# Kernel tuning notes

Hardware: AMD Instinct MI355X
Metric: run time of the kernel (lower is better)

## Reference

```python
import jax, jax.numpy as jnp
import numpy as np

N = 12        # ALL_QUBITS
COM_Q = 9     # COM_QUBITS
IMG_Q = 11    # IMG_QUBITS
LAYERS = 2
SQRT2 = float(np.sqrt(2.0))
H_GATE = jnp.asarray([[1.0, 1.0], [1.0, -1.0]], dtype=jnp.complex64) / SQRT2


def _bitrev_perm(q):
    # column j of the wires-1..q subspace corresponds to param index bitrev(j)
    idx = np.arange(2 ** q)
    rev = np.zeros_like(idx)
    for bpos in range(q):
        rev |= ((idx >> bpos) & 1) << (q - 1 - bpos)
    return rev


def _apply_1q(state, U, w):
    # state: (B, 2^N) complex; apply 2x2 gate U on wire w (wire 0 = MSB)
    B = state.shape[0]
    s = state.reshape(B, 2 ** w, 2, -1)
    return jnp.einsum('ij,bpjq->bpiq', U, s).reshape(B, -1)


def _apply_cnot(state, c, t):
    B = state.shape[0]
    s = state.reshape((B,) + (2,) * N)
    s0 = jax.lax.slice_in_dim(s, 0, 1, axis=c + 1)
    s1 = jnp.flip(jax.lax.slice_in_dim(s, 1, 2, axis=c + 1), axis=t + 1)
    return jnp.concatenate([s0, s1], axis=c + 1).reshape(B, -1)


def _frqi(state, angles, q):
    # Hadamards on wires 1..q, then uniformly-controlled RY(angles) on wire 0
    for w in range(1, q + 1):
        state = _apply_1q(state, H_GATE, w)
    rev = _bitrev_perm(q)
    half = 0.5 * angles[:, rev]            # (B, 2^q), angle per control column
    c = jnp.cos(half)[:, :, None]
    s = jnp.sin(half)[:, :, None]
    B = state.shape[0]
    st = state.reshape(B, 2, 2 ** q, -1)   # (B, wire0, wires1..q, rest)
    new0 = c * st[:, 0] - s * st[:, 1]
    new1 = s * st[:, 0] + c * st[:, 1]
    return jnp.stack([new0, new1], axis=1).reshape(B, -1)


def _rot(phi, theta, omega):
    # PennyLane Rot = RZ(omega) RY(theta) RZ(phi)
    c = jnp.cos(theta / 2)
    s = jnp.sin(theta / 2)
    m00 = jnp.exp(-0.5j * (phi + omega)) * c
    m01 = -jnp.exp(0.5j * (phi - omega)) * s
    m10 = jnp.exp(-0.5j * (phi - omega)) * s
    m11 = jnp.exp(0.5j * (phi + omega)) * c
    return jnp.stack([jnp.stack([m00, m01]), jnp.stack([m10, m11])])


def _circuit(com_params, img_params, qp):
    B = com_params.shape[0]
    state = jnp.zeros((B, 2 ** N), jnp.complex64).at[:, 0].set(1.0)
    state = _frqi(state, com_params, COM_Q)
    for l in range(LAYERS):  # StronglyEntanglingLayers
        for w in range(N):
            state = _apply_1q(state, _rot(qp[l, w, 0], qp[l, w, 1], qp[l, w, 2]), w)
        r = l % (N - 1) + 1  # default ranges
        for w in range(N):
            state = _apply_cnot(state, w, (w + r) % N)
    state = _frqi(state, img_params, IMG_Q)
    p = (jnp.abs(state.reshape(B, 2, -1)) ** 2).sum(axis=2)  # (B, 2) wire-0 probs
    return p[:, 1] - p[:, 0]  # expval of Hamiltonian = -1 * Z(0)


def setup_inputs() -> dict:
    key = jax.random.key(0)
    k1, k2, k3 = jax.random.split(key, 3)
    B = 1024
    x = jax.random.uniform(k1, (B, 2, 32, 32), dtype=jnp.float32)
    W = jax.random.normal(k2, (512, 2048), dtype=jnp.float32) * 0.02
    b = jnp.zeros((512,), dtype=jnp.float32)
    quantum_params = jax.random.uniform(k3, (LAYERS, N, 3), dtype=jnp.float32) * float(np.pi)
    return {"x": x, "W": W, "b": b, "quantum_params": quantum_params}


def reference(x, W, b, quantum_params):
    B = x.shape[0]
    xf = x.reshape(B, -1)                 # (B, 2048) img_params
    com = xf @ W.T + b                    # (B, 512) classical_nn output
    return _circuit(com, xf, quantum_params)
```

## Files before the change

kernel.cpp:

```cpp
#include <hip/hip_runtime.h>
#include <math.h>

#define RS2f 0.70710678118654752f

typedef __attribute__((ext_vector_type(8))) short bf16x8;
typedef __attribute__((ext_vector_type(4))) float f32x4;

__device__ __forceinline__ unsigned short f2bf(float f) {
    unsigned u = __float_as_uint(f);
    unsigned r = (u + 0x7fffu + ((u >> 16) & 1u)) >> 16;
    return (unsigned short)r;
}
__device__ __forceinline__ float bf2f(unsigned short h) {
    return __uint_as_float(((unsigned)h) << 16);
}

__global__ __launch_bounds__(256) void split_all(const float* __restrict__ x,
                                                 const float* __restrict__ W,
                                                 unsigned short* __restrict__ xc,
                                                 unsigned short* __restrict__ wc) {
    int idx = blockIdx.x * 256 + threadIdx.x;
    const float* src; unsigned short* dst;
    if (idx < 524288) { src = x; dst = xc; }
    else              { idx -= 524288; src = W; dst = wc; }
    int m = idx >> 9;
    int c4 = (idx & 511) << 2;
    const float4 v = *(const float4*)&src[m * 2048 + c4];
    ushort4 hi, lo;
    hi.x = f2bf(v.x); lo.x = f2bf(v.x - bf2f(hi.x));
    hi.y = f2bf(v.y); lo.y = f2bf(v.y - bf2f(hi.y));
    hi.z = f2bf(v.z); lo.z = f2bf(v.z - bf2f(hi.z));
    hi.w = f2bf(v.w); lo.w = f2bf(v.w - bf2f(hi.w));
    *(ushort4*)&dst[m * 4096 + c4] = hi;
    *(ushort4*)&dst[m * 4096 + 2048 + c4] = lo;
}

__global__ __launch_bounds__(256) void gemm64(const unsigned short* __restrict__ A,
                                              const unsigned short* __restrict__ B,
                                              float* __restrict__ P, int nch) {
    __shared__ short As[64 * 72];
    __shared__ short Bs[64 * 72];
    const int tid = threadIdx.x, lane = tid & 63, wv = tid >> 6;
    const int quad = lane >> 4, mrow = lane & 15;
    const int m0 = blockIdx.x * 64, n0 = blockIdx.y * 64;
    const int kb = blockIdx.z * nch * 64;
    const int srow = tid >> 2;
    const int sk = (tid & 3) * 16;
    const unsigned short* Arow = A + (size_t)(m0 + srow) * 4096 + kb + sk;
    const unsigned short* Brow = B + (size_t)(n0 + srow) * 4096 + kb + sk;

    f32x4 acc[4];
    #pragma unroll
    for (int j = 0; j < 4; ++j) acc[j] = (f32x4){0.f, 0.f, 0.f, 0.f};

    float4 a0 = *(const float4*)Arow;
    float4 a1 = *(const float4*)(Arow + 8);
    float4 b0 = *(const float4*)Brow;
    float4 b1 = *(const float4*)(Brow + 8);

    for (int ch = 0; ch < nch; ++ch) {
        __syncthreads();
        *(float4*)&As[srow * 72 + sk]     = a0;
        *(float4*)&As[srow * 72 + sk + 8] = a1;
        *(float4*)&Bs[srow * 72 + sk]     = b0;
        *(float4*)&Bs[srow * 72 + sk + 8] = b1;
        __syncthreads();
        if (ch + 1 < nch) {
            const int o = (ch + 1) * 64;
            a0 = *(const float4*)(Arow + o);
            a1 = *(const float4*)(Arow + o + 8);
            b0 = *(const float4*)(Brow + o);
            b1 = *(const float4*)(Brow + o + 8);
        }
        #pragma unroll
        for (int ks = 0; ks < 2; ++ks) {
            bf16x8 af = *(const bf16x8*)&As[(wv * 16 + mrow) * 72 + ks * 32 + quad * 8];
            #pragma unroll
            for (int j = 0; j < 4; ++j) {
                bf16x8 bf = *(const bf16x8*)&Bs[(j * 16 + mrow) * 72 + ks * 32 + quad * 8];
                acc[j] = __builtin_amdgcn_mfma_f32_16x16x32_bf16(af, bf, acc[j], 0, 0, 0);
            }
        }
    }
    float* Pz = P + (size_t)blockIdx.z * 524288;
    #pragma unroll
    for (int j = 0; j < 4; ++j)
        #pragma unroll
        for (int r = 0; r < 4; ++r)
            Pz[(m0 + wv * 16 + quad * 4 + r) * 512 + n0 + j * 16 + mrow] = acc[j][r];
}

__global__ __launch_bounds__(256) void gemm_f32(const float* __restrict__ A,
                                                const float* __restrict__ W,
                                                float* __restrict__ P) {
    __shared__ float Asf[32][128];
    __shared__ float Bsf[32][128];
    const int tid = threadIdx.x;
    const int m0 = blockIdx.x * 128;
    const int n0 = blockIdx.y * 128;
    const int kchunk = 2048 / gridDim.z;
    const int kbase = blockIdx.z * kchunk;
    const int tm = tid >> 4, tn = tid & 15;
    const int srow = tid >> 1;
    const int scol = (tid & 1) * 16;
    float acc[8][8] = {};
    for (int k0 = kbase; k0 < kbase + kchunk; k0 += 32) {
        float4 a[4], w[4];
        const float4* Ap = (const float4*)&A[(m0 + srow) * 2048 + k0 + scol];
        const float4* Wp = (const float4*)&W[(n0 + srow) * 2048 + k0 + scol];
        #pragma unroll
        for (int q = 0; q < 4; ++q) { a[q] = Ap[q]; w[q] = Wp[q]; }
        __syncthreads();
        #pragma unroll
        for (int q = 0; q < 4; ++q) {
            Asf[scol + 4*q + 0][srow] = a[q].x; Asf[scol + 4*q + 1][srow] = a[q].y;
            Asf[scol + 4*q + 2][srow] = a[q].z; Asf[scol + 4*q + 3][srow] = a[q].w;
            Bsf[scol + 4*q + 0][srow] = w[q].x; Bsf[scol + 4*q + 1][srow] = w[q].y;
            Bsf[scol + 4*q + 2][srow] = w[q].z; Bsf[scol + 4*q + 3][srow] = w[q].w;
        }
        __syncthreads();
        #pragma unroll
        for (int kk = 0; kk < 32; ++kk) {
            float4 af0 = *(const float4*)&Asf[kk][tm * 8];
            float4 af1 = *(const float4*)&Asf[kk][tm * 8 + 4];
            float4 bf0 = *(const float4*)&Bsf[kk][tn * 8];
            float4 bf1 = *(const float4*)&Bsf[kk][tn * 8 + 4];
            float av[8] = {af0.x,af0.y,af0.z,af0.w,af1.x,af1.y,af1.z,af1.w};
            float bv[8] = {bf0.x,bf0.y,bf0.z,bf0.w,bf1.x,bf1.y,bf1.z,bf1.w};
            #pragma unroll
            for (int r = 0; r < 8; ++r)
                #pragma unroll
                for (int c = 0; c < 8; ++c)
                    acc[r][c] += av[r] * bv[c];
        }
    }
    float* Pz = P + (size_t)blockIdx.z * 524288;
    #pragma unroll
    for (int r = 0; r < 8; ++r) {
        float4 lo = make_float4(acc[r][0], acc[r][1], acc[r][2], acc[r][3]);
        float4 hi = make_float4(acc[r][4], acc[r][5], acc[r][6], acc[r][7]);
        float* dst = &Pz[(m0 + tm*8 + r) * 512 + n0 + tn*8];
        *(float4*)dst = lo;
        *(float4*)(dst + 4) = hi;
    }
}

struct CMat { float m00r,m00i,m01r,m01i,m10r,m10i,m11r,m11i; };

__device__ __forceinline__ CMat mk_rot(const float* __restrict__ qp, int l, int w) {
    const float* g = qp + (l * 12 + w) * 3;
    float phi = g[0], th = g[1], om = g[2];
    float st, ct, sa, ca, sb, cb;
    sincosf(0.5f * th, &st, &ct);
    sincosf(0.5f * (phi + om), &sa, &ca);
    sincosf(0.5f * (phi - om), &sb, &cb);
    CMat M;
    M.m00r =  ct * ca; M.m00i = -ct * sa;
    M.m01r = -st * cb; M.m01i = -st * sb;
    M.m10r =  st * cb; M.m10i = -st * sb;
    M.m11r =  ct * ca; M.m11i =  ct * sa;
    return M;
}

template<int W> struct WI {
    static constexpr int kind = (W == 0 || W == 7) ? 2 : ((W >= 1 && W <= 6) ? 1 : 0);
    static constexpr int eb   = (W >= 8) ? (11 - W) : 0;
    static constexpr int lm   = (W >= 1 && W <= 6) ? (1 << (6 - W)) : 0;
    static constexpr int vm   = (W == 0) ? 2 : ((W == 7) ? 1 : 0);
};

__device__ __forceinline__ void exch_put(float* xbuf, int slot,
                                         const float vr[16], const float vi[16]) {
    __syncthreads();
    float4* p = (float4*)xbuf;
    #pragma unroll
    for (int j = 0; j < 8; ++j)
        p[(j << 8) + slot] = make_float4(vr[2*j], vi[2*j], vr[2*j+1], vi[2*j+1]);
    __syncthreads();
}

__device__ __forceinline__ void shfl_perm(float vr[16], float vi[16], int src) {
    #pragma unroll
    for (int e = 0; e < 16; ++e) {
        vr[e] = __shfl(vr[e], src, 64);
        vi[e] = __shfl(vi[e], src, 64);
    }
}

template<int EB>
__device__ __forceinline__ void rot_local(float vr[16], float vi[16], const CMat& M) {
    #pragma unroll
    for (int e = 0; e < 16; ++e) if (!(e & (1 << EB))) {
        const int e1 = e | (1 << EB);
        float x0r = vr[e],  x0i = vi[e];
        float x1r = vr[e1], x1i = vi[e1];
        vr[e]  = M.m00r*x0r - M.m00i*x0i + M.m01r*x1r - M.m01i*x1i;
        vi[e]  = M.m00r*x0i + M.m00i*x0r + M.m01r*x1i + M.m01i*x1r;
        vr[e1] = M.m10r*x0r - M.m10i*x0i + M.m11r*x1r - M.m11i*x1i;
        vi[e1] = M.m10r*x0i + M.m10i*x0r + M.m11r*x1i + M.m11i*x1r;
    }
}

template<int LM>
__device__ __forceinline__ void rot_lane(float vr[16], float vi[16], int lane, const CMat& M) {
    const bool hi = lane & LM;
    const float Ar = hi ? M.m11r : M.m00r, Ai = hi ? M.m11i : M.m00i;
    const float Br = hi ? M.m10r : M.m01r, Bi = hi ? M.m10i : M.m01i;
    #pragma unroll
    for (int e = 0; e < 16; ++e) {
        float pr = __shfl_xor(vr[e], LM, 64);
        float pi = __shfl_xor(vi[e], LM, 64);
        float orr = vr[e], oi = vi[e];
        vr[e] = Ar*orr - Ai*oi + Br*pr - Bi*pi;
        vi[e] = Ar*oi + Ai*orr + Br*pi + Bi*pr;
    }
}

template<int VM>
__device__ __forceinline__ void rot_wave(float vr[16], float vi[16], float* xbuf,
                                         int waveId, int lane, const CMat& M) {
    exch_put(xbuf, (waveId << 6) + lane, vr, vi);
    const float4* p = (const float4*)xbuf;
    const int ps = ((waveId ^ VM) << 6) + lane;
    const bool hi = waveId & VM;
    const float Ar = hi ? M.m11r : M.m00r, Ai = hi ? M.m11i : M.m00i;
    const float Br = hi ? M.m10r : M.m01r, Bi = hi ? M.m10i : M.m01i;
    #pragma unroll
    for (int j = 0; j < 8; ++j) {
        float4 q = p[(j << 8) + ps];
        const int e0 = 2*j, e1 = 2*j + 1;
        float r0 = vr[e0], i0 = vi[e0], r1 = vr[e1], i1 = vi[e1];
        vr[e0] = Ar*r0 - Ai*i0 + Br*q.x - Bi*q.y;
        vi[e0] = Ar*i0 + Ai*r0 + Br*q.y + Bi*q.x;
        vr[e1] = Ar*r1 - Ai*i1 + Br*q.z - Bi*q.w;
        vi[e1] = Ar*i1 + Ai*r1 + Br*q.w + Bi*q.z;
    }
}

template<int W>
__device__ __forceinline__ void rot_wire(float vr[16], float vi[16], float* xbuf,
                                         int waveId, int lane, const CMat& M) {
    if constexpr (WI<W>::kind == 0)      rot_local<WI<W>::eb>(vr, vi, M);
    else if constexpr (WI<W>::kind == 1) rot_lane<WI<W>::lm>(vr, vi, lane, M);
    else                                 rot_wave<WI<W>::vm>(vr, vi, xbuf, waveId, lane, M);
}

template<int C, int T>
__device__ __forceinline__ void cnot(float vr[16], float vi[16], float* xbuf,
                                     int waveId, int lane) {
    constexpr int ck = WI<C>::kind, tk = WI<T>::kind;
    if constexpr (ck == 0 && tk == 0) {
        constexpr int cb = 1 << WI<C>::eb, tb = 1 << WI<T>::eb;
        #pragma unroll
        for (int e = 0; e < 16; ++e) if ((e & cb) && !(e & tb)) {
            const int e1 = e | tb;
            float t = vr[e]; vr[e] = vr[e1]; vr[e1] = t;
            t = vi[e]; vi[e] = vi[e1]; vi[e1] = t;
        }
    } else if constexpr (ck == 0 && tk == 1) {
        constexpr int cb = 1 << WI<C>::eb, tm = WI<T>::lm;
        #pragma unroll
        for (int e = 0; e < 16; ++e) if (e & cb) {
            vr[e] = __shfl_xor(vr[e], tm, 64);
            vi[e] = __shfl_xor(vi[e], tm, 64);
        }
    } else if constexpr (ck == 0 && tk == 2) {
        constexpr int cb = 1 << WI<C>::eb, vm = WI<T>::vm;
        exch_put(xbuf, (waveId << 6) + lane, vr, vi);
        const float4* p = (const float4*)xbuf;
        const int ps = ((waveId ^ vm) << 6) + lane;
        #pragma unroll
        for (int j = 0; j < 8; ++j) {
            if ((((2*j) & cb) != 0) || (((2*j+1) & cb) != 0)) {
                float4 q = p[(j << 8) + ps];
                if (((2*j) & cb) != 0)   { vr[2*j]   = q.x; vi[2*j]   = q.y; }
                if (((2*j+1) & cb) != 0) { vr[2*j+1] = q.z; vi[2*j+1] = q.w; }
            }
        }
    } else if constexpr (ck == 1 && tk == 0) {
        constexpr int cm = WI<C>::lm, tb = 1 << WI<T>::eb;
        const bool cc = lane & cm;
        #pragma unroll
        for (int e = 0; e < 16; ++e) if (!(e & tb)) {
            const int e1 = e | tb;
            float a = vr[e], bb = vr[e1];
            vr[e] = cc ? bb : a; vr[e1] = cc ? a : bb;
            a = vi[e]; bb = vi[e1];
            vi[e] = cc ? bb : a; vi[e1] = cc ? a : bb;
        }
    } else if constexpr (ck == 1 && tk == 1) {
        constexpr int cm = WI<C>::lm, tm = WI<T>::lm;
        const int src = (lane & cm) ? (lane ^ tm) : lane;
        shfl_perm(vr, vi, src);
    } else if constexpr (ck == 1 && tk == 2) {
        constexpr int cm = WI<C>::lm, vm = WI<T>::vm;
        exch_put(xbuf, (waveId << 6) + lane, vr, vi);
        const float4* p = (const float4*)xbuf;
        const int ps = ((waveId ^ vm) << 6) + lane;
        const bool take = lane & cm;
        #pragma unroll
        for (int j = 0; j < 8; ++j) {
            float4 q = p[(j << 8) + ps];
            vr[2*j]   = take ? q.x : vr[2*j];   vi[2*j]   = take ? q.y : vi[2*j];
            vr[2*j+1] = take ? q.z : vr[2*j+1]; vi[2*j+1] = take ? q.w : vi[2*j+1];
        }
    } else if constexpr (ck == 2 && tk == 0) {
        constexpr int vm = WI<C>::vm, tb = 1 << WI<T>::eb;
        if (waveId & vm) {
            #pragma unroll
            for (int e = 0; e < 16; ++e) if (!(e & tb)) {
                const int e1 = e | tb;
                float t = vr[e]; vr[e] = vr[e1]; vr[e1] = t;
                t = vi[e]; vi[e] = vi[e1]; vi[e1] = t;
            }
        }
    } else {
        constexpr int vm = WI<C>::vm, tm = WI<T>::lm;
        if (waveId & vm) {
            #pragma unroll
            for (int e = 0; e < 16; ++e) {
                vr[e] = __shfl_xor(vr[e], tm, 64);
                vi[e] = __shfl_xor(vi[e], tm, 64);
            }
        }
    }
}

template<int W>
__device__ __forceinline__ void h_wire(float vr[16], float vi[16], float* xbuf,
                                       int waveId, int lane) {
    if constexpr (WI<W>::kind == 0) {
        constexpr int tb = 1 << WI<W>::eb;
        #pragma unroll
        for (int e = 0; e < 16; ++e) if (!(e & tb)) {
            const int e1 = e | tb;
            float x0 = vr[e], x1 = vr[e1];
            vr[e] = (x0 + x1) * RS2f; vr[e1] = (x0 - x1) * RS2f;
            x0 = vi[e]; x1 = vi[e1];
            vi[e] = (x0 + x1) * RS2f; vi[e1] = (x0 - x1) * RS2f;
        }
    } else if constexpr (WI<W>::kind == 1) {
        constexpr int m = WI<W>::lm;
        const float sgn = (lane & m) ? -RS2f : RS2f;
        #pragma unroll
        for (int e = 0; e < 16; ++e) {
            float pr = __shfl_xor(vr[e], m, 64);
            float pi = __shfl_xor(vi[e], m, 64);
            vr[e] = pr * RS2f + vr[e] * sgn;
            vi[e] = pi * RS2f + vi[e] * sgn;
        }
    } else {
        constexpr int vm = WI<W>::vm;
        exch_put(xbuf, (waveId << 6) + lane, vr, vi);
        const float4* p = (const float4*)xbuf;
        const int ps = ((waveId ^ vm) << 6) + lane;
        const float sgn = (waveId & vm) ? -RS2f : RS2f;
        #pragma unroll
        for (int j = 0; j < 8; ++j) {
            float4 q = p[(j << 8) + ps];
            vr[2*j]   = q.x * RS2f + vr[2*j]   * sgn;
            vi[2*j]   = q.y * RS2f + vi[2*j]   * sgn;
            vr[2*j+1] = q.z * RS2f + vr[2*j+1] * sgn;
            vi[2*j+1] = q.w * RS2f + vi[2*j+1] * sgn;
        }
    }
}

__global__ __launch_bounds__(256) void circuit_kernel(const float* __restrict__ P,
                                                      const float* __restrict__ bias,
                                                      const float* __restrict__ xf,
                                                      const float* __restrict__ qp,
                                                      float* __restrict__ out, int SK) {
    __shared__ float xbuf[8192];
    __shared__ float ang[2048];
    const int tid = threadIdx.x;
    const int lane = tid & 63;
    const int waveId = tid >> 6;
    const int b = blockIdx.x;

    if (tid < 128) {
        float4 s = ((const float4*)bias)[tid];
        for (int z = 0; z < SK; ++z) {
            float4 p4 = *(const float4*)&P[(size_t)z * 524288 + b * 512 + tid * 4];
            s.x += p4.x; s.y += p4.y; s.z += p4.z; s.w += p4.w;
        }
        ((float4*)ang)[tid] = s;
    }
    __syncthreads();

    float vr[16], vi[16];
    #pragma unroll
    for (int e = 0; e < 16; ++e) { vr[e] = 0.0f; vi[e] = 0.0f; }

    const float K9 = 0.044194173824159216f;
    #pragma unroll
    for (int m = 0; m < 4; ++m) {
        int j = (lane << 3) | ((waveId & 1) << 2) | m;
        int rj = (int)(__brev((unsigned)j) >> 23);
        float s, c;
        sincosf(0.5f * ang[rj], &s, &c);
        vr[m << 2] = K9 * ((waveId & 2) ? s : c);
    }

    #pragma unroll 1
    for (int l = 0; l < 2; ++l) {
        { CMat M = mk_rot(qp, l, 0);  rot_wire<0 >(vr, vi, xbuf, waveId, lane, M); }
        { CMat M = mk_rot(qp, l, 1);  rot_wire<1 >(vr, vi, xbuf, waveId, lane, M); }
        { CMat M = mk_rot(qp, l, 2);  rot_wire<2 >(vr, vi, xbuf, waveId, lane, M); }
        { CMat M = mk_rot(qp, l, 3);  rot_wire<3 >(vr, vi, xbuf, waveId, lane, M); }
        { CMat M = mk_rot(qp, l, 4);  rot_wire<4 >(vr, vi, xbuf, waveId, lane, M); }
        { CMat M = mk_rot(qp, l, 5);  rot_wire<5 >(vr, vi, xbuf, waveId, lane, M); }
        { CMat M = mk_rot(qp, l, 6);  rot_wire<6 >(vr, vi, xbuf, waveId, lane, M); }
        { CMat M = mk_rot(qp, l, 7);  rot_wire<7 >(vr, vi, xbuf, waveId, lane, M); }
        { CMat M = mk_rot(qp, l, 8);  rot_wire<8 >(vr, vi, xbuf, waveId, lane, M); }
        { CMat M = mk_rot(qp, l, 9);  rot_wire<9 >(vr, vi, xbuf, waveId, lane, M); }
        { CMat M = mk_rot(qp, l, 10); rot_wire<10>(vr, vi, xbuf, waveId, lane, M); }
        { CMat M = mk_rot(qp, l, 11); rot_wire<11>(vr, vi, xbuf, waveId, lane, M); }
        if (l == 0) {
            int j = lane;
            j ^= (j & 2)  ? 1  : 0;
            j ^= (j & 4)  ? 2  : 0;
            j ^= (j & 8)  ? 4  : 0;
            j ^= (j & 16) ? 8  : 0;
            j ^= (j & 32) ? 16 : 0;
            j ^= (waveId & 2) ? 32 : 0;
            shfl_perm(vr, vi, j);
            cnot<6,7>(vr,vi,xbuf,waveId,lane);   cnot<7,8>(vr,vi,xbuf,waveId,lane);
            cnot<8,9>(vr,vi,xbuf,waveId,lane);   cnot<9,10>(vr,vi,xbuf,waveId,lane);
            cnot<10,11>(vr,vi,xbuf,waveId,lane); cnot<11,0>(vr,vi,xbuf,waveId,lane);
        } else {
            int j = lane;
            j ^= (j & 4)  ? 1  : 0;
            j ^= (j & 8)  ? 2  : 0;
            j ^= (j & 16) ? 4  : 0;
            j ^= (j & 32) ? 8  : 0;
            j ^= (waveId & 2) ? 16 : 0;
            shfl_perm(vr, vi, j);
            cnot<5,7>(vr,vi,xbuf,waveId,lane);   cnot<6,8>(vr,vi,xbuf,waveId,lane);
            cnot<7,9>(vr,vi,xbuf,waveId,lane);   cnot<8,10>(vr,vi,xbuf,waveId,lane);
            cnot<9,11>(vr,vi,xbuf,waveId,lane);  cnot<10,0>(vr,vi,xbuf,waveId,lane);
            cnot<11,1>(vr,vi,xbuf,waveId,lane);
        }
    }

    h_wire<1>(vr,vi,xbuf,waveId,lane);  h_wire<2>(vr,vi,xbuf,waveId,lane);
    h_wire<3>(vr,vi,xbuf,waveId,lane);  h_wire<4>(vr,vi,xbuf,waveId,lane);
    h_wire<5>(vr,vi,xbuf,waveId,lane);  h_wire<6>(vr,vi,xbuf,waveId,lane);
    h_wire<7>(vr,vi,xbuf,waveId,lane);  h_wire<8>(vr,vi,xbuf,waveId,lane);
    h_wire<9>(vr,vi,xbuf,waveId,lane);  h_wire<10>(vr,vi,xbuf,waveId,lane);
    h_wire<11>(vr,vi,xbuf,waveId,lane);

    {
        const float4* x4 = (const float4*)(xf + b * 2048);
        ((float4*)ang)[tid]       = x4[tid];
        ((float4*)ang)[tid + 256] = x4[tid + 256];
    }
    __syncthreads();

    exch_put(xbuf, (waveId << 6) + lane, vr, vi);
    {
        const float4* p = (const float4*)xbuf;
        const int ps = ((waveId ^ 2) << 6) + lane;
        const bool hi = waveId & 2;
        float acc = 0.0f;
        #pragma unroll
        for (int j = 0; j < 8; ++j) {
            float4 q = p[(j << 8) + ps];
            #pragma unroll
            for (int h = 0; h < 2; ++h) {
                const int e = 2*j + h;
                const float prr = h ? q.z : q.x;
                const float pii = h ? q.w : q.y;
                int v = (lane << 5) | ((waveId & 1) << 4) | e;
                int rv = (int)(__brev((unsigned)v) >> 21);
                float s, c;
                sincosf(0.5f * ang[rv], &s, &c);
                float nr = hi ? (s*prr + c*vr[e]) : (c*vr[e] - s*prr);
                float ni = hi ? (s*pii + c*vi[e]) : (c*vi[e] - s*pii);
                acc += nr*nr + ni*ni;
            }
        }
        if (!hi) acc = -acc;
        #pragma unroll
        for (int off = 32; off > 0; off >>= 1) acc += __shfl_down(acc, off, 64);
        __syncthreads();
        if (lane == 0) xbuf[waveId] = acc;
        __syncthreads();
        if (tid == 0) out[b] = xbuf[0] + xbuf[1] + xbuf[2] + xbuf[3];
    }
}

extern "C" void kernel_launch(void* const* d_in, const int* in_sizes, int n_in,
                              void* d_out, int out_size, void* d_ws, size_t ws_size,
                              hipStream_t stream) {
    const float* x    = (const float*)d_in[0];
    const float* W    = (const float*)d_in[1];
    const float* bias = (const float*)d_in[2];
    const float* qp   = (const float*)d_in[3];
    float* out = (float*)d_out;

    const size_t MB = 1024ull * 1024;
    const size_t BASE = 12 * MB;
    if (ws_size >= BASE + 4 * MB) {
        unsigned short* xc = (unsigned short*)d_ws;
        unsigned short* wc = (unsigned short*)((char*)d_ws + 8 * MB);
        float* P = (float*)((char*)d_ws + BASE);
        int SK;
        if      (ws_size >= BASE + 16 * MB) SK = 8;
        else if (ws_size >= BASE + 8 * MB)  SK = 4;
        else                                SK = 2;
        split_all<<<3072, 256, 0, stream>>>(x, W, xc, wc);
        dim3 g(16, 8, SK);
        gemm64<<<g, 256, 0, stream>>>(xc, wc, P, 4096 / SK / 64);
        circuit_kernel<<<1024, 256, 0, stream>>>(P, bias, x, qp, out, SK);
    } else {
        float* P = (float*)d_ws;
        const size_t slab = 1024 * 512 * sizeof(float);
        int SK = 1;
        if      (ws_size >= 16 * slab) SK = 16;
        else if (ws_size >=  8 * slab) SK = 8;
        else if (ws_size >=  4 * slab) SK = 4;
        else if (ws_size >=  2 * slab) SK = 2;
        dim3 ggrid(8, 4, SK);
        gemm_f32<<<ggrid, 256, 0, stream>>>(x, W, P);
        circuit_kernel<<<1024, 256, 0, stream>>>(P, bias, x, qp, out, SK);
    }
}
```

Measured before the change: 150.5 us.

## Fuse split, GEMM and circuit into one cooperative persistent kernel

Merges the bf16 split conversion, the split-K MFMA GEMM and the per-sample circuit simulation into a single cooperative kernel, separated by grid-wide syncs, with shared memory reused across the phases. Split-K is fixed at 4 and work is distributed with grid-stride loops over 256 or 512 blocks, chosen from the occupancy query. The goal is to remove the launch gaps between three kernels. In exchange it adds grid barrier costs, and the circuit phase now runs on fewer resident blocks than the original 1024. The fallback path is rewritten as a smaller fp32 GEMM that adds the bias, followed by a standalone circuit kernel.

```diff
diff --git a/kernel.cpp b/kernel.cpp
--- a/kernel.cpp
+++ b/kernel.cpp
@@ -1,5 +1,8 @@
 #include <hip/hip_runtime.h>
+#include <hip/hip_cooperative_groups.h>
 #include <math.h>
+
+namespace cg = cooperative_groups;
 
 #define RS2f 0.70710678118654752f
 
@@ -13,136 +16,6 @@
 }
 __device__ __forceinline__ float bf2f(unsigned short h) {
     return __uint_as_float(((unsigned)h) << 16);
-}
-
-__global__ __launch_bounds__(256) void split_all(const float* __restrict__ x,
-                                                 const float* __restrict__ W,
-                                                 unsigned short* __restrict__ xc,
-                                                 unsigned short* __restrict__ wc) {
-    int idx = blockIdx.x * 256 + threadIdx.x;
-    const float* src; unsigned short* dst;
-    if (idx < 524288) { src = x; dst = xc; }
-    else              { idx -= 524288; src = W; dst = wc; }
-    int m = idx >> 9;
-    int c4 = (idx & 511) << 2;
-    const float4 v = *(const float4*)&src[m * 2048 + c4];
-    ushort4 hi, lo;
-    hi.x = f2bf(v.x); lo.x = f2bf(v.x - bf2f(hi.x));
-    hi.y = f2bf(v.y); lo.y = f2bf(v.y - bf2f(hi.y));
-    hi.z = f2bf(v.z); lo.z = f2bf(v.z - bf2f(hi.z));
-    hi.w = f2bf(v.w); lo.w = f2bf(v.w - bf2f(hi.w));
-    *(ushort4*)&dst[m * 4096 + c4] = hi;
-    *(ushort4*)&dst[m * 4096 + 2048 + c4] = lo;
-}
-
-__global__ __launch_bounds__(256) void gemm64(const unsigned short* __restrict__ A,
-                                              const unsigned short* __restrict__ B,
-                                              float* __restrict__ P, int nch) {
-    __shared__ short As[64 * 72];
-    __shared__ short Bs[64 * 72];
-    const int tid = threadIdx.x, lane = tid & 63, wv = tid >> 6;
-    const int quad = lane >> 4, mrow = lane & 15;
-    const int m0 = blockIdx.x * 64, n0 = blockIdx.y * 64;
-    const int kb = blockIdx.z * nch * 64;
-    const int srow = tid >> 2;
-    const int sk = (tid & 3) * 16;
-    const unsigned short* Arow = A + (size_t)(m0 + srow) * 4096 + kb + sk;
-    const unsigned short* Brow = B + (size_t)(n0 + srow) * 4096 + kb + sk;
-
-    f32x4 acc[4];
-    #pragma unroll
-    for (int j = 0; j < 4; ++j) acc[j] = (f32x4){0.f, 0.f, 0.f, 0.f};
-
-    float4 a0 = *(const float4*)Arow;
-    float4 a1 = *(const float4*)(Arow + 8);
-    float4 b0 = *(const float4*)Brow;
-    float4 b1 = *(const float4*)(Brow + 8);
-
-    for (int ch = 0; ch < nch; ++ch) {
-        __syncthreads();
-        *(float4*)&As[srow * 72 + sk]     = a0;
-        *(float4*)&As[srow * 72 + sk + 8] = a1;
-        *(float4*)&Bs[srow * 72 + sk]     = b0;
-        *(float4*)&Bs[srow * 72 + sk + 8] = b1;
-        __syncthreads();
-        if (ch + 1 < nch) {
-            const int o = (ch + 1) * 64;
-            a0 = *(const float4*)(Arow + o);
-            a1 = *(const float4*)(Arow + o + 8);
-            b0 = *(const float4*)(Brow + o);
-            b1 = *(const float4*)(Brow + o + 8);
-        }
-        #pragma unroll
-        for (int ks = 0; ks < 2; ++ks) {
-            bf16x8 af = *(const bf16x8*)&As[(wv * 16 + mrow) * 72 + ks * 32 + quad * 8];
-            #pragma unroll
-            for (int j = 0; j < 4; ++j) {
-                bf16x8 bf = *(const bf16x8*)&Bs[(j * 16 + mrow) * 72 + ks * 32 + quad * 8];
-                acc[j] = __builtin_amdgcn_mfma_f32_16x16x32_bf16(af, bf, acc[j], 0, 0, 0);
-            }
-        }
-    }
-    float* Pz = P + (size_t)blockIdx.z * 524288;
-    #pragma unroll
-    for (int j = 0; j < 4; ++j)
-        #pragma unroll
-        for (int r = 0; r < 4; ++r)
-            Pz[(m0 + wv * 16 + quad * 4 + r) * 512 + n0 + j * 16 + mrow] = acc[j][r];
-}
-
-__global__ __launch_bounds__(256) void gemm_f32(const float* __restrict__ A,
-                                                const float* __restrict__ W,
-                                                float* __restrict__ P) {
-    __shared__ float Asf[32][128];
-    __shared__ float Bsf[32][128];
-    const int tid = threadIdx.x;
-    const int m0 = blockIdx.x * 128;
-    const int n0 = blockIdx.y * 128;
-    const int kchunk = 2048 / gridDim.z;
-    const int kbase = blockIdx.z * kchunk;
-    const int tm = tid >> 4, tn = tid & 15;
-    const int srow = tid >> 1;
-    const int scol = (tid & 1) * 16;
-    float acc[8][8] = {};
-    for (int k0 = kbase; k0 < kbase + kchunk; k0 += 32) {
-        float4 a[4], w[4];
-        const float4* Ap = (const float4*)&A[(m0 + srow) * 2048 + k0 + scol];
-        const float4* Wp = (const float4*)&W[(n0 + srow) * 2048 + k0 + scol];
-        #pragma unroll
-        for (int q = 0; q < 4; ++q) { a[q] = Ap[q]; w[q] = Wp[q]; }
-        __syncthreads();
-        #pragma unroll
-        for (int q = 0; q < 4; ++q) {
-            Asf[scol + 4*q + 0][srow] = a[q].x; Asf[scol + 4*q + 1][srow] = a[q].y;
-            Asf[scol + 4*q + 2][srow] = a[q].z; Asf[scol + 4*q + 3][srow] = a[q].w;
-            Bsf[scol + 4*q + 0][srow] = w[q].x; Bsf[scol + 4*q + 1][srow] = w[q].y;
-            Bsf[scol + 4*q + 2][srow] = w[q].z; Bsf[scol + 4*q + 3][srow] = w[q].w;
-        }
-        __syncthreads();
-        #pragma unroll
-        for (int kk = 0; kk < 32; ++kk) {
-            float4 af0 = *(const float4*)&Asf[kk][tm * 8];
-            float4 af1 = *(const float4*)&Asf[kk][tm * 8 + 4];
-            float4 bf0 = *(const float4*)&Bsf[kk][tn * 8];
-            float4 bf1 = *(const float4*)&Bsf[kk][tn * 8 + 4];
-            float av[8] = {af0.x,af0.y,af0.z,af0.w,af1.x,af1.y,af1.z,af1.w};
-            float bv[8] = {bf0.x,bf0.y,bf0.z,bf0.w,bf1.x,bf1.y,bf1.z,bf1.w};
-            #pragma unroll
-            for (int r = 0; r < 8; ++r)
-                #pragma unroll
-                for (int c = 0; c < 8; ++c)
-                    acc[r][c] += av[r] * bv[c];
-        }
-    }
-    float* Pz = P + (size_t)blockIdx.z * 524288;
-    #pragma unroll
-    for (int r = 0; r < 8; ++r) {
-        float4 lo = make_float4(acc[r][0], acc[r][1], acc[r][2], acc[r][3]);
-        float4 hi = make_float4(acc[r][4], acc[r][5], acc[r][6], acc[r][7]);
-        float* dst = &Pz[(m0 + tm*8 + r) * 512 + n0 + tn*8];
-        *(float4*)dst = lo;
-        *(float4*)(dst + 4) = hi;
-    }
 }
 
 struct CMat { float m00r,m00i,m01r,m01i,m10r,m10i,m11r,m11i; };
@@ -366,32 +239,268 @@
     }
 }
 
-__global__ __launch_bounds__(256) void circuit_kernel(const float* __restrict__ P,
-                                                      const float* __restrict__ bias,
-                                                      const float* __restrict__ xf,
-                                                      const float* __restrict__ qp,
-                                                      float* __restrict__ out, int SK) {
-    __shared__ float xbuf[8192];
-    __shared__ float ang[2048];
+__global__ __launch_bounds__(256) void fused_all(const float* __restrict__ x,
+                                                 const float* __restrict__ W,
+                                                 const float* __restrict__ bias,
+                                                 const float* __restrict__ qp,
+                                                 unsigned short* __restrict__ xc,
+                                                 unsigned short* __restrict__ wc,
+                                                 float* __restrict__ P,
+                                                 float* __restrict__ out) {
+    __shared__ float smem[10240];
+    float* xbuf = smem;
+    float* ang  = smem + 8192;
+    short* As   = (short*)smem;
+    short* Bs   = (short*)smem + 4608;
+
     const int tid = threadIdx.x;
     const int lane = tid & 63;
     const int waveId = tid >> 6;
+    const int nblk = gridDim.x;
+    cg::grid_group grid = cg::this_grid();
+
+    for (int idx = blockIdx.x * 256 + tid; idx < 786432; idx += nblk * 256) {
+        int i2 = idx;
+        const float* src; unsigned short* dst;
+        if (i2 < 524288) { src = x; dst = xc; }
+        else             { i2 -= 524288; src = W; dst = wc; }
+        int m = i2 >> 9;
+        int c4 = (i2 & 511) << 2;
+        const float4 v = *(const float4*)&src[m * 2048 + c4];
+        ushort4 hi, lo;
+        hi.x = f2bf(v.x); lo.x = f2bf(v.x - bf2f(hi.x));
+        hi.y = f2bf(v.y); lo.y = f2bf(v.y - bf2f(hi.y));
+        hi.z = f2bf(v.z); lo.z = f2bf(v.z - bf2f(hi.z));
+        hi.w = f2bf(v.w); lo.w = f2bf(v.w - bf2f(hi.w));
+        *(ushort4*)&dst[m * 4096 + c4] = hi;
+        *(ushort4*)&dst[m * 4096 + 2048 + c4] = lo;
+    }
+    __threadfence();
+    grid.sync();
+
+    for (int t = blockIdx.x; t < 512; t += nblk) {
+        const int m0 = (t & 15) * 64, n0 = ((t >> 4) & 7) * 64, z = t >> 7;
+        const int kb = z * 1024;
+        const int quad = lane >> 4, mrow = lane & 15;
+        const int srow = tid >> 2;
+        const int sk = (tid & 3) * 16;
+        const unsigned short* Arow = xc + (size_t)(m0 + srow) * 4096 + kb + sk;
+        const unsigned short* Brow = wc + (size_t)(n0 + srow) * 4096 + kb + sk;
+        f32x4 acc[4];
+        #pragma unroll
+        for (int j = 0; j < 4; ++j) acc[j] = (f32x4){0.f, 0.f, 0.f, 0.f};
+        float4 a0 = *(const float4*)Arow;
+        float4 a1 = *(const float4*)(Arow + 8);
+        float4 b0 = *(const float4*)Brow;
+        float4 b1 = *(const float4*)(Brow + 8);
+        for (int ch = 0; ch < 16; ++ch) {
+            __syncthreads();
+            *(float4*)&As[srow * 72 + sk]     = a0;
+            *(float4*)&As[srow * 72 + sk + 8] = a1;
+            *(float4*)&Bs[srow * 72 + sk]     = b0;
+            *(float4*)&Bs[srow * 72 + sk + 8] = b1;
+            __syncthreads();
+            if (ch + 1 < 16) {
+                const int o = (ch + 1) * 64;
+                a0 = *(const float4*)(Arow + o);
+                a1 = *(const float4*)(Arow + o + 8);
+                b0 = *(const float4*)(Brow + o);
+                b1 = *(const float4*)(Brow + o + 8);
+            }
+            #pragma unroll
+            for (int ks = 0; ks < 2; ++ks) {
+                bf16x8 af = *(const bf16x8*)&As[(waveId * 16 + mrow) * 72 + ks * 32 + quad * 8];
+                #pragma unroll
+                for (int j = 0; j < 4; ++j) {
+                    bf16x8 bf = *(const bf16x8*)&Bs[(j * 16 + mrow) * 72 + ks * 32 + quad * 8];
+                    acc[j] = __builtin_amdgcn_mfma_f32_16x16x32_bf16(af, bf, acc[j], 0, 0, 0);
+                }
+            }
+        }
+        float* Pz = P + (size_t)z * 524288;
+        #pragma unroll
+        for (int j = 0; j < 4; ++j)
+            #pragma unroll
+            for (int r = 0; r < 4; ++r)
+                Pz[(m0 + waveId * 16 + quad * 4 + r) * 512 + n0 + j * 16 + mrow] = acc[j][r];
+        __syncthreads();
+    }
+    __threadfence();
+    grid.sync();
+
+    for (int b = blockIdx.x; b < 1024; b += nblk) {
+        __syncthreads();
+
+        if (tid < 128) {
+            float4 s = ((const float4*)bias)[tid];
+            #pragma unroll
+            for (int z = 0; z < 4; ++z) {
+                float4 p4 = *(const float4*)&P[(size_t)z * 524288 + b * 512 + tid * 4];
+                s.x += p4.x; s.y += p4.y; s.z += p4.z; s.w += p4.w;
+            }
+            ((float4*)ang)[tid] = s;
+        }
+        __syncthreads();
+
+        float vr[16], vi[16];
+        #pragma unroll
+        for (int e = 0; e < 16; ++e) { vr[e] = 0.0f; vi[e] = 0.0f; }
+
+        const float K9 = 0.044194173824159216f;
+        #pragma unroll
+        for (int m = 0; m < 4; ++m) {
+            int j = (lane << 3) | ((waveId & 1) << 2) | m;
+            int rj = (int)(__brev((unsigned)j) >> 23);
+            float s, c;
+            sincosf(0.5f * ang[rj], &s, &c);
+            vr[m << 2] = K9 * ((waveId & 2) ? s : c);
+        }
+
+        #pragma unroll 1
+        for (int l = 0; l < 2; ++l) {
+            { CMat M = mk_rot(qp, l, 0);  rot_wire<0 >(vr, vi, xbuf, waveId, lane, M); }
+            { CMat M = mk_rot(qp, l, 1);  rot_wire<1 >(vr, vi, xbuf, waveId, lane, M); }
+            { CMat M = mk_rot(qp, l, 2);  rot_wire<2 >(vr, vi, xbuf, waveId, lane, M); }
+            { CMat M = mk_rot(qp, l, 3);  rot_wire<3 >(vr, vi, xbuf, waveId, lane, M); }
+            { CMat M = mk_rot(qp, l, 4);  rot_wire<4 >(vr, vi, xbuf, waveId, lane, M); }
+            { CMat M = mk_rot(qp, l, 5);  rot_wire<5 >(vr, vi, xbuf, waveId, lane, M); }
+            { CMat M = mk_rot(qp, l, 6);  rot_wire<6 >(vr, vi, xbuf, waveId, lane, M); }
+            { CMat M = mk_rot(qp, l, 7);  rot_wire<7 >(vr, vi, xbuf, waveId, lane, M); }
+            { CMat M = mk_rot(qp, l, 8);  rot_wire<8 >(vr, vi, xbuf, waveId, lane, M); }
+            { CMat M = mk_rot(qp, l, 9);  rot_wire<9 >(vr, vi, xbuf, waveId, lane, M); }
+            { CMat M = mk_rot(qp, l, 10); rot_wire<10>(vr, vi, xbuf, waveId, lane, M); }
+            { CMat M = mk_rot(qp, l, 11); rot_wire<11>(vr, vi, xbuf, waveId, lane, M); }
+            if (l == 0) {
+                int j = lane;
+                j ^= (j & 2)  ? 1  : 0;
+                j ^= (j & 4)  ? 2  : 0;
+                j ^= (j & 8)  ? 4  : 0;
+                j ^= (j & 16) ? 8  : 0;
+                j ^= (j & 32) ? 16 : 0;
+                j ^= (waveId & 2) ? 32 : 0;
+                shfl_perm(vr, vi, j);
+                cnot<6,7>(vr,vi,xbuf,waveId,lane);   cnot<7,8>(vr,vi,xbuf,waveId,lane);
+                cnot<8,9>(vr,vi,xbuf,waveId,lane);   cnot<9,10>(vr,vi,xbuf,waveId,lane);
+                cnot<10,11>(vr,vi,xbuf,waveId,lane); cnot<11,0>(vr,vi,xbuf,waveId,lane);
+            } else {
+                int j = lane;
+                j ^= (j & 4)  ? 1  : 0;
+                j ^= (j & 8)  ? 2  : 0;
+                j ^= (j & 16) ? 4  : 0;
+                j ^= (j & 32) ? 8  : 0;
+                j ^= (waveId & 2) ? 16 : 0;
+                shfl_perm(vr, vi, j);
+                cnot<5,7>(vr,vi,xbuf,waveId,lane);   cnot<6,8>(vr,vi,xbuf,waveId,lane);
+                cnot<7,9>(vr,vi,xbuf,waveId,lane);   cnot<8,10>(vr,vi,xbuf,waveId,lane);
+                cnot<9,11>(vr,vi,xbuf,waveId,lane);  cnot<10,0>(vr,vi,xbuf,waveId,lane);
+                cnot<11,1>(vr,vi,xbuf,waveId,lane);
+            }
+        }
+
+        h_wire<1>(vr,vi,xbuf,waveId,lane);  h_wire<2>(vr,vi,xbuf,waveId,lane);
+        h_wire<3>(vr,vi,xbuf,waveId,lane);  h_wire<4>(vr,vi,xbuf,waveId,lane);
+        h_wire<5>(vr,vi,xbuf,waveId,lane);  h_wire<6>(vr,vi,xbuf,waveId,lane);
+        h_wire<7>(vr,vi,xbuf,waveId,lane);  h_wire<8>(vr,vi,xbuf,waveId,lane);
+        h_wire<9>(vr,vi,xbuf,waveId,lane);  h_wire<10>(vr,vi,xbuf,waveId,lane);
+        h_wire<11>(vr,vi,xbuf,waveId,lane);
+
+        {
+            const float4* x4 = (const float4*)(x + b * 2048);
+            ((float4*)ang)[tid]       = x4[tid];
+            ((float4*)ang)[tid + 256] = x4[tid + 256];
+        }
+        __syncthreads();
+
+        exch_put(xbuf, (waveId << 6) + lane, vr, vi);
+        {
+            const float4* p = (const float4*)xbuf;
+            const int ps = ((waveId ^ 2) << 6) + lane;
+            const bool hi = waveId & 2;
+            float acc = 0.0f;
+            #pragma unroll
+            for (int j = 0; j < 8; ++j) {
+                float4 q = p[(j << 8) + ps];
+                #pragma unroll
+                for (int h = 0; h < 2; ++h) {
+                    const int e = 2*j + h;
+                    const float prr = h ? q.z : q.x;
+                    const float pii = h ? q.w : q.y;
+                    int v = (lane << 5) | ((waveId & 1) << 4) | e;
+                    int rv = (int)(__brev((unsigned)v) >> 21);
+                    float s, c;
+                    sincosf(0.5f * ang[rv], &s, &c);
+                    float nr = hi ? (s*prr + c*vr[e]) : (c*vr[e] - s*prr);
+                    float ni = hi ? (s*pii + c*vi[e]) : (c*vi[e] - s*pii);
+                    acc += nr*nr + ni*ni;
+                }
+            }
+            if (!hi) acc = -acc;
+            #pragma unroll
+            for (int off = 32; off > 0; off >>= 1) acc += __shfl_down(acc, off, 64);
+            __syncthreads();
+            if (lane == 0) xbuf[waveId] = acc;
+            __syncthreads();
+            if (tid == 0) out[b] = xbuf[0] + xbuf[1] + xbuf[2] + xbuf[3];
+        }
+    }
+}
+
+__global__ __launch_bounds__(256) void gemm_f32(const float* __restrict__ A,
+                                                const float* __restrict__ W,
+                                                const float* __restrict__ bias,
+                                                float* __restrict__ C) {
+    __shared__ float Asf[64][33];
+    __shared__ float Bsf[32][33];
+    const int tid = threadIdx.x;
+    const int m0 = blockIdx.x * 64;
+    const int n0 = blockIdx.y * 32;
+    const int tm = tid >> 4, tn = tid & 15;
+    float acc[4][2] = {};
+    for (int k0 = 0; k0 < 2048; k0 += 32) {
+        #pragma unroll
+        for (int i = 0; i < 8; ++i) {
+            int idx = tid + i * 256;
+            Asf[idx >> 5][idx & 31] = A[(m0 + (idx >> 5)) * 2048 + k0 + (idx & 31)];
+        }
+        #pragma unroll
+        for (int i = 0; i < 4; ++i) {
+            int idx = tid + i * 256;
+            Bsf[idx >> 5][idx & 31] = W[(n0 + (idx >> 5)) * 2048 + k0 + (idx & 31)];
+        }
+        __syncthreads();
+        #pragma unroll
+        for (int kk = 0; kk < 32; ++kk) {
+            float a0 = Asf[tm*4+0][kk], a1 = Asf[tm*4+1][kk];
+            float a2 = Asf[tm*4+2][kk], a3 = Asf[tm*4+3][kk];
+            float b0 = Bsf[tn*2+0][kk], b1 = Bsf[tn*2+1][kk];
+            acc[0][0] += a0*b0; acc[0][1] += a0*b1;
+            acc[1][0] += a1*b0; acc[1][1] += a1*b1;
+            acc[2][0] += a2*b0; acc[2][1] += a2*b1;
+            acc[3][0] += a3*b0; acc[3][1] += a3*b1;
+        }
+        __syncthreads();
+    }
+    #pragma unroll
+    for (int r = 0; r < 4; ++r)
+        #pragma unroll
+        for (int c = 0; c < 2; ++c)
+            C[(m0 + tm*4 + r) * 512 + n0 + tn*2 + c] = acc[r][c] + bias[n0 + tn*2 + c];
+}
+
+__global__ __launch_bounds__(256) void circuit_sa(const float* __restrict__ com,
+                                                  const float* __restrict__ xf,
+                                                  const float* __restrict__ qp,
+                                                  float* __restrict__ out) {
+    __shared__ float smem[10240];
+    float* xbuf = smem;
+    float* ang  = smem + 8192;
+    const int tid = threadIdx.x, lane = tid & 63, waveId = tid >> 6;
     const int b = blockIdx.x;
-
-    if (tid < 128) {
-        float4 s = ((const float4*)bias)[tid];
-        for (int z = 0; z < SK; ++z) {
-            float4 p4 = *(const float4*)&P[(size_t)z * 524288 + b * 512 + tid * 4];
-            s.x += p4.x; s.y += p4.y; s.z += p4.z; s.w += p4.w;
-        }
-        ((float4*)ang)[tid] = s;
-    }
+    if (tid < 128) ((float4*)ang)[tid] = ((const float4*)(com + b * 512))[tid];
     __syncthreads();
-
     float vr[16], vi[16];
     #pragma unroll
     for (int e = 0; e < 16; ++e) { vr[e] = 0.0f; vi[e] = 0.0f; }
-
     const float K9 = 0.044194173824159216f;
     #pragma unroll
     for (int m = 0; m < 4; ++m) {
@@ -401,7 +510,6 @@
         sincosf(0.5f * ang[rj], &s, &c);
         vr[m << 2] = K9 * ((waveId & 2) ? s : c);
     }
-
     #pragma unroll 1
     for (int l = 0; l < 2; ++l) {
         { CMat M = mk_rot(qp, l, 0);  rot_wire<0 >(vr, vi, xbuf, waveId, lane, M); }
@@ -418,22 +526,17 @@
         { CMat M = mk_rot(qp, l, 11); rot_wire<11>(vr, vi, xbuf, waveId, lane, M); }
         if (l == 0) {
             int j = lane;
-            j ^= (j & 2)  ? 1  : 0;
-            j ^= (j & 4)  ? 2  : 0;
-            j ^= (j & 8)  ? 4  : 0;
-            j ^= (j & 16) ? 8  : 0;
-            j ^= (j & 32) ? 16 : 0;
-            j ^= (waveId & 2) ? 32 : 0;
+            j ^= (j & 2)  ? 1  : 0;  j ^= (j & 4)  ? 2  : 0;
+            j ^= (j & 8)  ? 4  : 0;  j ^= (j & 16) ? 8  : 0;
+            j ^= (j & 32) ? 16 : 0;  j ^= (waveId & 2) ? 32 : 0;
             shfl_perm(vr, vi, j);
             cnot<6,7>(vr,vi,xbuf,waveId,lane);   cnot<7,8>(vr,vi,xbuf,waveId,lane);
             cnot<8,9>(vr,vi,xbuf,waveId,lane);   cnot<9,10>(vr,vi,xbuf,waveId,lane);
             cnot<10,11>(vr,vi,xbuf,waveId,lane); cnot<11,0>(vr,vi,xbuf,waveId,lane);
         } else {
             int j = lane;
-            j ^= (j & 4)  ? 1  : 0;
-            j ^= (j & 8)  ? 2  : 0;
-            j ^= (j & 16) ? 4  : 0;
-            j ^= (j & 32) ? 8  : 0;
+            j ^= (j & 4)  ? 1  : 0;  j ^= (j & 8)  ? 2  : 0;
+            j ^= (j & 16) ? 4  : 0;  j ^= (j & 32) ? 8  : 0;
             j ^= (waveId & 2) ? 16 : 0;
             shfl_perm(vr, vi, j);
             cnot<5,7>(vr,vi,xbuf,waveId,lane);   cnot<6,8>(vr,vi,xbuf,waveId,lane);
@@ -442,21 +545,18 @@
             cnot<11,1>(vr,vi,xbuf,waveId,lane);
         }
     }
-
     h_wire<1>(vr,vi,xbuf,waveId,lane);  h_wire<2>(vr,vi,xbuf,waveId,lane);
     h_wire<3>(vr,vi,xbuf,waveId,lane);  h_wire<4>(vr,vi,xbuf,waveId,lane);
     h_wire<5>(vr,vi,xbuf,waveId,lane);  h_wire<6>(vr,vi,xbuf,waveId,lane);
     h_wire<7>(vr,vi,xbuf,waveId,lane);  h_wire<8>(vr,vi,xbuf,waveId,lane);
     h_wire<9>(vr,vi,xbuf,waveId,lane);  h_wire<10>(vr,vi,xbuf,waveId,lane);
     h_wire<11>(vr,vi,xbuf,waveId,lane);
-
     {
         const float4* x4 = (const float4*)(xf + b * 2048);
         ((float4*)ang)[tid]       = x4[tid];
         ((float4*)ang)[tid + 256] = x4[tid + 256];
     }
     __syncthreads();
-
     exch_put(xbuf, (waveId << 6) + lane, vr, vi);
     {
         const float4* p = (const float4*)xbuf;
@@ -500,29 +600,22 @@
     float* out = (float*)d_out;
 
     const size_t MB = 1024ull * 1024;
-    const size_t BASE = 12 * MB;
-    if (ws_size >= BASE + 4 * MB) {
+    int occ = 0;
+    (void)hipOccupancyMaxActiveBlocksPerMultiprocessor(&occ, fused_all, 256, 0);
+
+    if (ws_size >= 20 * MB && occ >= 1) {
         unsigned short* xc = (unsigned short*)d_ws;
         unsigned short* wc = (unsigned short*)((char*)d_ws + 8 * MB);
-        float* P = (float*)((char*)d_ws + BASE);
-        int SK;
-        if      (ws_size >= BASE + 16 * MB) SK = 8;
-        else if (ws_size >= BASE + 8 * MB)  SK = 4;
-        else                                SK = 2;
-        split_all<<<3072, 256, 0, stream>>>(x, W, xc, wc);
-        dim3 g(16, 8, SK);
-        gemm64<<<g, 256, 0, stream>>>(xc, wc, P, 4096 / SK / 64);
-        circuit_kernel<<<1024, 256, 0, stream>>>(P, bias, x, qp, out, SK);
+        float* P = (float*)((char*)d_ws + 12 * MB);
+        int nblk = (occ >= 2) ? 512 : 256;
+        void* args[] = {(void*)&x, (void*)&W, (void*)&bias, (void*)&qp,
+                        (void*)&xc, (void*)&wc, (void*)&P, (void*)&out};
+        hipLaunchCooperativeKernel((const void*)fused_all, dim3(nblk), dim3(256),
+                                   args, 0, stream);
     } else {
-        float* P = (float*)d_ws;
-        const size_t slab = 1024 * 512 * sizeof(float);
-        int SK = 1;
-        if      (ws_size >= 16 * slab) SK = 16;
-        else if (ws_size >=  8 * slab) SK = 8;
-        else if (ws_size >=  4 * slab) SK = 4;
-        else if (ws_size >=  2 * slab) SK = 2;
-        dim3 ggrid(8, 4, SK);
-        gemm_f32<<<ggrid, 256, 0, stream>>>(x, W, P);
-        circuit_kernel<<<1024, 256, 0, stream>>>(P, bias, x, qp, out, SK);
-    }
-}
+        float* com = (float*)d_ws;
+        dim3 g(16, 16);
+        gemm_f32<<<g, 256, 0, stream>>>(x, W, bias, com);
+        circuit_sa<<<1024, 256, 0, stream>>>(com, x, qp, out);
+    }
+}
```

Result: slower. 323.5 us (+114.9%).
